# Performance work log

Hardware: AMD Instinct MI355X
Metric: run time of the kernel (lower is better)

Reference implementation:

```python
import math
import jax, jax.numpy as jnp
import numpy as np

B, S, D = 4, 2048, 1024
NEG = -1e20

def setup_inputs() -> dict:
    key = jax.random.key(0)
    k1, k2, k3, k4 = jax.random.split(key, 4)
    X = jax.random.normal(k1, (B, S, D), dtype=jnp.float32)
    # True = masked position (masked_fill semantics)
    attention_mask = jax.random.randint(k2, (B, S, S), 0, 2).astype(bool)
    scale = 1.0 / math.sqrt(D)
    W_qkv = jax.random.normal(k3, (D, 3 * D), dtype=jnp.float32) * scale
    b_qkv = jnp.zeros((3 * D,), dtype=jnp.float32)
    W_out = jax.random.normal(k4, (D, D), dtype=jnp.float32) * scale
    b_out = jnp.zeros((D,), dtype=jnp.float32)
    return {"X": X, "attention_mask": attention_mask,
            "W_qkv": W_qkv, "b_qkv": b_qkv, "W_out": W_out, "b_out": b_out}

def reference(X, attention_mask, W_qkv, b_qkv, W_out, b_out):
    dim = X.shape[-1]
    QKV = X @ W_qkv + b_qkv                      # [B,S,3D]
    Q, K, V = jnp.split(QKV, 3, axis=-1)         # each [B,S,D]
    scores = jnp.einsum('bqd,bkd->bqk', Q, K) / math.sqrt(dim)  # [B,S,S]
    scores = jnp.where(attention_mask, NEG, scores)
    attn = jax.nn.softmax(scores, axis=-1)       # dropout_rate=0.0 -> identity
    ctx = jnp.einsum('bqk,bkd->bqd', attn, V)    # [B,S,D]
    return ctx @ W_out + b_out
```

## Files before the change

kernel.cpp:

```cpp
#include <hip/hip_runtime.h>
#include <cstdint>
#include <cstddef>

#define BB 4
#define SS 2048
#define DD 1024

typedef _Float16 f16;
typedef _Float16 f16x8 __attribute__((ext_vector_type(8)));
typedef _Float16 f16x4 __attribute__((ext_vector_type(4)));
typedef float fx4 __attribute__((ext_vector_type(4)));

__device__ __forceinline__ void async_copy16(void* lds, const void* g) {
  __builtin_amdgcn_global_load_lds(
      (__attribute__((address_space(1))) void*)const_cast<void*>(g),
      (__attribute__((address_space(3))) void*)lds,
      16, 0, 0);
}

enum { EPI_BIAS = 0, EPI_MASKEXP = 1, EPI_ROWSCALE = 2, EPI_QKV = 3 };

template <typename OutT, int MODE>
__global__ __launch_bounds__(256, 2) void gemm_nt(
    const f16* __restrict__ A, long long strideA, int lda,
    const f16* __restrict__ Bt, long long strideB, int ldb,
    OutT* __restrict__ C, long long strideC, int ldc,
    const float* __restrict__ bias, const int* __restrict__ mask,
    float* __restrict__ rowSum, f16* __restrict__ vt, float scale, int K) {
  __shared__ __align__(16) char smem[32768];

  const int t = threadIdx.x;
  const int lane = t & 63;
  const int wid = t >> 6;
  const long long bz = blockIdx.z;
  const int tileM = blockIdx.y * 128;
  const int tileN = blockIdx.x * 128;

  const f16* Ab = A + bz * strideA;
  const f16* Bb = Bt + bz * strideB;
  OutT* Cb = C + bz * strideC;

  const int sr = t >> 2;
  const int sc = (((t & 3) ^ ((t >> 3) & 3)) * 8);
  const f16* pa0 = Ab + (size_t)(tileM + sr) * lda + sc;
  const f16* pa1 = Ab + (size_t)(tileM + 64 + sr) * lda + sc;
  const f16* pb0 = Bb + (size_t)(tileN + sr) * ldb + sc;
  const f16* pb1 = Bb + (size_t)(tileN + 64 + sr) * ldb + sc;
  const int tb = t * 16;

  const int waveM = (wid >> 1) * 64;
  const int waveN = (wid & 1) * 64;
  const int r16 = lane & 15;
  const int quad = lane >> 4;
  const int sw = (r16 >> 1) & 3;

  fx4 acc[4][4] = {};

  const int nIter = K >> 5;
  {
    char* b0 = smem;
    async_copy16(b0 + tb, pa0);
    async_copy16(b0 + 4096 + tb, pa1);
    async_copy16(b0 + 8192 + tb, pb0);
    async_copy16(b0 + 12288 + tb, pb1);
  }

#pragma unroll 2
  for (int i = 0; i < nIter; ++i) {
    __syncthreads();
    if (i + 1 < nIter) {
      char* nb = smem + ((i + 1) & 1) * 16384;
      const int k = (i + 1) << 5;
      async_copy16(nb + tb, pa0 + k);
      async_copy16(nb + 4096 + tb, pa1 + k);
      async_copy16(nb + 8192 + tb, pb0 + k);
      async_copy16(nb + 12288 + tb, pb1 + k);
    }
    const f16* As = (const f16*)(smem + (i & 1) * 16384);
    const f16* Bs = As + 4096;

    f16x8 af[4], bf[4];
#pragma unroll
    for (int x = 0; x < 4; ++x)
      af[x] = *(const f16x8*)&As[(waveM + x * 16 + r16) * 32 + (quad ^ sw) * 8];
#pragma unroll
    for (int x = 0; x < 4; ++x)
      bf[x] = *(const f16x8*)&Bs[(waveN + x * 16 + r16) * 32 + (quad ^ sw) * 8];

#pragma unroll
    for (int x = 0; x < 4; ++x)
#pragma unroll
      for (int j = 0; j < 4; ++j)
        acc[x][j] =
            __builtin_amdgcn_mfma_f32_16x16x32_f16(af[x], bf[j], acc[x][j], 0, 0, 0);
  }

  if constexpr (MODE == EPI_BIAS) {
#pragma unroll
    for (int j = 0; j < 4; ++j) {
      const int col = tileN + waveN + j * 16 + r16;
      const float bv = bias[col];
#pragma unroll
      for (int i = 0; i < 4; ++i) {
#pragma unroll
        for (int r = 0; r < 4; ++r) {
          const int row = tileM + waveM + i * 16 + quad * 4 + r;
          Cb[(size_t)row * ldc + col] = (OutT)(acc[i][j][r] * scale + bv);
        }
      }
    }
  } else if constexpr (MODE == EPI_QKV) {
    if (tileN < 2 * DD) {
#pragma unroll
      for (int j = 0; j < 4; ++j) {
        const int col = tileN + waveN + j * 16 + r16;
        const float bv = bias[col];
#pragma unroll
        for (int i = 0; i < 4; ++i) {
#pragma unroll
          for (int r = 0; r < 4; ++r) {
            const int row = tileM + waveM + i * 16 + quad * 4 + r;
            Cb[(size_t)row * ldc + col] = (OutT)(acc[i][j][r] + bv);
          }
        }
      }
    } else {
      const int b = tileM >> 11;
      const int s0 = (tileM & 2047) + waveM;
      f16* vb = vt + (size_t)b * DD * SS;
#pragma unroll
      for (int j = 0; j < 4; ++j) {
        const int col = tileN + waveN + j * 16 + r16;
        const float bv = bias[col];
        const int d = col - 2 * DD;
#pragma unroll
        for (int i = 0; i < 4; ++i) {
          const int s = s0 + i * 16 + quad * 4;
          f16x4 v4;
#pragma unroll
          for (int r = 0; r < 4; ++r) v4[r] = (f16)(acc[i][j][r] + bv);
          *(f16x4*)&vb[(size_t)d * SS + s] = v4;
        }
      }
    }
  } else if constexpr (MODE == EPI_MASKEXP) {
    uint8_t* lm = (uint8_t*)smem;
    const int* maskb = mask + bz * (long long)SS * SS;
#pragma unroll
    for (int it = 0; it < 16; ++it) {
      const int f = it * 256 + t;
      const int r = f >> 5;
      const int q = f & 31;
      const int4 mv =
          *(const int4*)&maskb[(size_t)(tileM + r) * SS + tileN + q * 4];
      uchar4 mb;
      mb.x = mv.x ? 1 : 0;
      mb.y = mv.y ? 1 : 0;
      mb.z = mv.z ? 1 : 0;
      mb.w = mv.w ? 1 : 0;
      const int c4 = (q * 4) ^ (((r >> 2) & 3) * 32);
      *(uchar4*)&lm[r * 128 + c4] = mb;
    }
    __syncthreads();

#pragma unroll
    for (int i = 0; i < 4; ++i) {
#pragma unroll
      for (int r = 0; r < 4; ++r) {
        const int lr = waveM + i * 16 + quad * 4 + r;
        const int row = tileM + lr;
        const int swm = ((lr >> 2) & 3) * 32;
        float part = 0.0f;
#pragma unroll
        for (int j = 0; j < 4; ++j) {
          const int lc = waveN + j * 16 + r16;
          const int mv = lm[lr * 128 + (lc ^ swm)];
          const float e = mv ? 0.0f : __expf(acc[i][j][r] * scale);
          Cb[(size_t)row * ldc + tileN + lc] = (OutT)e;
          part += e;
        }
#pragma unroll
        for (int d = 1; d < 16; d <<= 1) part += __shfl_xor(part, d, 64);
        if (r16 == 0) atomicAdd(&rowSum[bz * SS + row], part);
      }
    }
  } else {
#pragma unroll
    for (int i = 0; i < 4; ++i) {
#pragma unroll
      for (int r = 0; r < 4; ++r) {
        const int row = tileM + waveM + i * 16 + quad * 4 + r;
        const float inv = scale / rowSum[bz * SS + row];
#pragma unroll
        for (int j = 0; j < 4; ++j) {
          const int col = tileN + waveN + j * 16 + r16;
          Cb[(size_t)row * ldc + col] = (OutT)(acc[i][j][r] * inv);
        }
      }
    }
  }
}

__global__ __launch_bounds__(256) void k_conv(const float* __restrict__ in,
                                              f16* __restrict__ out, int n4) {
  const int i = blockIdx.x * 256 + threadIdx.x;
  if (i >= n4) return;
  const float4 v = ((const float4*)in)[i];
  f16x4 h = {(f16)v.x, (f16)v.y, (f16)v.z, (f16)v.w};
  ((f16x4*)out)[i] = h;
}

__global__ __launch_bounds__(256) void k_zero(float* __restrict__ p, int n) {
  const int i = blockIdx.x * 256 + threadIdx.x;
  if (i < n) p[i] = 0.0f;
}

__global__ __launch_bounds__(256) void k_transpose_conv(const float* __restrict__ in,
                                                        f16* __restrict__ out, int R,
                                                        int C) {
  __shared__ float tile[32][33];
  const int bx = blockIdx.x * 32;
  const int by = blockIdx.y * 32;
  const int tx = threadIdx.x;
  const int ty = threadIdx.y;
  for (int i = ty; i < 32; i += 8)
    tile[i][tx] = in[(size_t)(by + i) * C + bx + tx];
  __syncthreads();
  for (int i = ty; i < 32; i += 8)
    out[(size_t)(bx + i) * R + by + tx] = (f16)tile[tx][i];
}

extern "C" void kernel_launch(void* const* d_in, const int* in_sizes, int n_in,
                              void* d_out, int out_size, void* d_ws, size_t ws_size,
                              hipStream_t stream) {
  const float* X = (const float*)d_in[0];
  const int* mask = (const int*)d_in[1];
  const float* Wqkv = (const float*)d_in[2];
  const float* bqkv = (const float*)d_in[3];
  const float* Wout = (const float*)d_in[4];
  const float* bout = (const float*)d_in[5];
  float* out = (float*)d_out;

  char* ws = (char*)d_ws;
  f16* Xh = (f16*)(ws + 0);
  f16* Wqkvt = (f16*)(ws + 16777216);
  f16* Woutt = (f16*)(ws + 23068672);
  f16* QK = (f16*)(ws + 25165824);
  f16* Vt = (f16*)(ws + 58720256);
  f16* E = (f16*)(ws + 75497472);
  f16* Ctx = (f16*)(ws + 109051904);
  float* rowSum = (float*)(ws + 125829120);

  k_conv<<<dim3(8192), dim3(256), 0, stream>>>(X, Xh, 8388608 / 4);
  k_transpose_conv<<<dim3(96, 32), dim3(32, 8), 0, stream>>>(Wqkv, Wqkvt, DD, 3 * DD);
  k_transpose_conv<<<dim3(32, 32), dim3(32, 8), 0, stream>>>(Wout, Woutt, DD, DD);
  k_zero<<<dim3(32), dim3(256), 0, stream>>>(rowSum, BB * SS);

  gemm_nt<f16, EPI_QKV><<<dim3(24, 64, 1), dim3(256), 0, stream>>>(
      Xh, 0LL, DD, Wqkvt, 0LL, DD, QK, 0LL, 2 * DD, bqkv, nullptr, nullptr, Vt,
      1.0f, DD);

  gemm_nt<f16, EPI_MASKEXP><<<dim3(16, 16, 4), dim3(256), 0, stream>>>(
      QK, (long long)SS * 2 * DD, 2 * DD, QK + DD, (long long)SS * 2 * DD, 2 * DD,
      E, (long long)SS * SS, SS, nullptr, mask, rowSum, nullptr, 0.03125f, DD);

  gemm_nt<f16, EPI_ROWSCALE><<<dim3(8, 16, 4), dim3(256), 0, stream>>>(
      E, (long long)SS * SS, SS, Vt, (long long)DD * SS, SS, Ctx,
      (long long)SS * DD, DD, nullptr, nullptr, rowSum, nullptr, 1.0f, SS);

  gemm_nt<float, EPI_BIAS><<<dim3(8, 64, 1), dim3(256), 0, stream>>>(
      Ctx, 0LL, DD, Woutt, 0LL, DD, out, 0LL, DD, bout, nullptr, nullptr, nullptr,
      1.0f, DD);
}
```

Before: 356.3 us.

## Replace LDS double-buffered GEMM staging with direct global-to-register prefetch

The GEMM main loop no longer stages A/B tiles through LDS with async global_load_lds and barriers. Each wave now loads its MFMA fragments straight from global memory into registers and prefetches the next K slice, with K made a template parameter so the loop fully unrolls. This removes the LDS traffic and __syncthreads per iteration. In exchange, each wave fetches its own A/B rows, so A rows are read once by each of the two waves sharing them (same for B), losing the block-level reuse. It also uses 16-byte strided row loads that coalesce poorly, raises register pressure, and drops the occupancy hint of two blocks per CU.

New measurement: 631.7 us. +77.3%, slower.

```diff
diff --git a/kernel.cpp b/kernel.cpp
--- a/kernel.cpp
+++ b/kernel.cpp
@@ -11,24 +11,15 @@
 typedef _Float16 f16x4 __attribute__((ext_vector_type(4)));
 typedef float fx4 __attribute__((ext_vector_type(4)));
 
-__device__ __forceinline__ void async_copy16(void* lds, const void* g) {
-  __builtin_amdgcn_global_load_lds(
-      (__attribute__((address_space(1))) void*)const_cast<void*>(g),
-      (__attribute__((address_space(3))) void*)lds,
-      16, 0, 0);
-}
-
 enum { EPI_BIAS = 0, EPI_MASKEXP = 1, EPI_ROWSCALE = 2, EPI_QKV = 3 };
 
-template <typename OutT, int MODE>
-__global__ __launch_bounds__(256, 2) void gemm_nt(
+template <typename OutT, int MODE, int K_ITERS>
+__global__ __launch_bounds__(256) void gemm_nt(
     const f16* __restrict__ A, long long strideA, int lda,
     const f16* __restrict__ Bt, long long strideB, int ldb,
     OutT* __restrict__ C, long long strideC, int ldc,
     const float* __restrict__ bias, const int* __restrict__ mask,
-    float* __restrict__ rowSum, f16* __restrict__ vt, float scale, int K) {
-  __shared__ __align__(16) char smem[32768];
-
+    float* __restrict__ rowSum, f16* __restrict__ vt, float scale) {
   const int t = threadIdx.x;
   const int lane = t & 63;
   const int wid = t >> 6;
@@ -40,59 +31,50 @@
   const f16* Bb = Bt + bz * strideB;
   OutT* Cb = C + bz * strideC;
 
-  const int sr = t >> 2;
-  const int sc = (((t & 3) ^ ((t >> 3) & 3)) * 8);
-  const f16* pa0 = Ab + (size_t)(tileM + sr) * lda + sc;
-  const f16* pa1 = Ab + (size_t)(tileM + 64 + sr) * lda + sc;
-  const f16* pb0 = Bb + (size_t)(tileN + sr) * ldb + sc;
-  const f16* pb1 = Bb + (size_t)(tileN + 64 + sr) * ldb + sc;
-  const int tb = t * 16;
-
   const int waveM = (wid >> 1) * 64;
   const int waveN = (wid & 1) * 64;
   const int r16 = lane & 15;
   const int quad = lane >> 4;
-  const int sw = (r16 >> 1) & 3;
+
+  const f16* pA[4];
+  const f16* pB[4];
+#pragma unroll
+  for (int x = 0; x < 4; ++x) {
+    pA[x] = Ab + (size_t)(tileM + waveM + x * 16 + r16) * lda + quad * 8;
+    pB[x] = Bb + (size_t)(tileN + waveN + x * 16 + r16) * ldb + quad * 8;
+  }
 
   fx4 acc[4][4] = {};
 
-  const int nIter = K >> 5;
-  {
-    char* b0 = smem;
-    async_copy16(b0 + tb, pa0);
-    async_copy16(b0 + 4096 + tb, pa1);
-    async_copy16(b0 + 8192 + tb, pb0);
-    async_copy16(b0 + 12288 + tb, pb1);
-  }
-
-#pragma unroll 2
-  for (int i = 0; i < nIter; ++i) {
-    __syncthreads();
-    if (i + 1 < nIter) {
-      char* nb = smem + ((i + 1) & 1) * 16384;
-      const int k = (i + 1) << 5;
-      async_copy16(nb + tb, pa0 + k);
-      async_copy16(nb + 4096 + tb, pa1 + k);
-      async_copy16(nb + 8192 + tb, pb0 + k);
-      async_copy16(nb + 12288 + tb, pb1 + k);
-    }
-    const f16* As = (const f16*)(smem + (i & 1) * 16384);
-    const f16* Bs = As + 4096;
-
-    f16x8 af[4], bf[4];
-#pragma unroll
-    for (int x = 0; x < 4; ++x)
-      af[x] = *(const f16x8*)&As[(waveM + x * 16 + r16) * 32 + (quad ^ sw) * 8];
-#pragma unroll
-    for (int x = 0; x < 4; ++x)
-      bf[x] = *(const f16x8*)&Bs[(waveN + x * 16 + r16) * 32 + (quad ^ sw) * 8];
-
+  f16x8 a0[4], b0[4];
+#pragma unroll
+  for (int x = 0; x < 4; ++x) {
+    a0[x] = *(const f16x8*)(pA[x]);
+    b0[x] = *(const f16x8*)(pB[x]);
+  }
+
+#pragma unroll
+  for (int i = 0; i < K_ITERS; ++i) {
+    f16x8 a1[4], b1[4];
+    if (i + 1 < K_ITERS) {
+      const int k = (i + 1) * 32;
+#pragma unroll
+      for (int x = 0; x < 4; ++x) {
+        a1[x] = *(const f16x8*)(pA[x] + k);
+        b1[x] = *(const f16x8*)(pB[x] + k);
+      }
+    }
 #pragma unroll
     for (int x = 0; x < 4; ++x)
 #pragma unroll
       for (int j = 0; j < 4; ++j)
         acc[x][j] =
-            __builtin_amdgcn_mfma_f32_16x16x32_f16(af[x], bf[j], acc[x][j], 0, 0, 0);
+            __builtin_amdgcn_mfma_f32_16x16x32_f16(a0[x], b0[j], acc[x][j], 0, 0, 0);
+#pragma unroll
+    for (int x = 0; x < 4; ++x) {
+      a0[x] = a1[x];
+      b0[x] = b1[x];
+    }
   }
 
   if constexpr (MODE == EPI_BIAS) {
@@ -144,7 +126,7 @@
       }
     }
   } else if constexpr (MODE == EPI_MASKEXP) {
-    uint8_t* lm = (uint8_t*)smem;
+    __shared__ uint8_t lm[16384];
     const int* maskb = mask + bz * (long long)SS * SS;
 #pragma unroll
     for (int it = 0; it < 16; ++it) {
@@ -256,19 +238,19 @@
   k_transpose_conv<<<dim3(32, 32), dim3(32, 8), 0, stream>>>(Wout, Woutt, DD, DD);
   k_zero<<<dim3(32), dim3(256), 0, stream>>>(rowSum, BB * SS);
 
-  gemm_nt<f16, EPI_QKV><<<dim3(24, 64, 1), dim3(256), 0, stream>>>(
+  gemm_nt<f16, EPI_QKV, 32><<<dim3(24, 64, 1), dim3(256), 0, stream>>>(
       Xh, 0LL, DD, Wqkvt, 0LL, DD, QK, 0LL, 2 * DD, bqkv, nullptr, nullptr, Vt,
-      1.0f, DD);
-
-  gemm_nt<f16, EPI_MASKEXP><<<dim3(16, 16, 4), dim3(256), 0, stream>>>(
+      1.0f);
+
+  gemm_nt<f16, EPI_MASKEXP, 32><<<dim3(16, 16, 4), dim3(256), 0, stream>>>(
       QK, (long long)SS * 2 * DD, 2 * DD, QK + DD, (long long)SS * 2 * DD, 2 * DD,
-      E, (long long)SS * SS, SS, nullptr, mask, rowSum, nullptr, 0.03125f, DD);
-
-  gemm_nt<f16, EPI_ROWSCALE><<<dim3(8, 16, 4), dim3(256), 0, stream>>>(
+      E, (long long)SS * SS, SS, nullptr, mask, rowSum, nullptr, 0.03125f);
+
+  gemm_nt<f16, EPI_ROWSCALE, 64><<<dim3(8, 16, 4), dim3(256), 0, stream>>>(
       E, (long long)SS * SS, SS, Vt, (long long)DD * SS, SS, Ctx,
-      (long long)SS * DD, DD, nullptr, nullptr, rowSum, nullptr, 1.0f, SS);
-
-  gemm_nt<float, EPI_BIAS><<<dim3(8, 64, 1), dim3(256), 0, stream>>>(
+      (long long)SS * DD, DD, nullptr, nullptr, rowSum, nullptr, 1.0f);
+
+  gemm_nt<float, EPI_BIAS, 32><<<dim3(8, 64, 1), dim3(256), 0, stream>>>(
       Ctx, 0LL, DD, Woutt, 0LL, DD, out, 0LL, DD, bout, nullptr, nullptr, nullptr,
-      1.0f, DD);
-}
+      1.0f);
+}
```
